# Performance work log

Measured on AMD Instinct MI355X. Metric: run time of the kernel, lower is better.

The kernel has to match this reference:

```python
import jax, jax.numpy as jnp
import numpy as np

B, L, D, H, T = 64, 512, 768, 384, 9  # batch, seq_len, hidden, hidden//2, num_tags


def setup_inputs() -> dict:
    key = jax.random.key(0)
    ks = jax.random.split(key, 8)
    return {
        "encoder_out": jax.random.normal(ks[0], (B, L, D), jnp.float32),
        "ner_labels": jax.random.randint(ks[1], (B, L), 0, T),
        "mask": jnp.ones((B, L), jnp.bool_),
        "W1": jax.random.normal(ks[2], (D, H), jnp.float32) / np.sqrt(D).astype(np.float32),
        "b1": jnp.zeros((H,), jnp.float32),
        "W2": jax.random.normal(ks[3], (H, T), jnp.float32) / np.sqrt(H).astype(np.float32),
        "b2": jnp.zeros((T,), jnp.float32),
        "start_trans": jax.random.uniform(ks[4], (T,), jnp.float32, -0.1, 0.1),
        "end_trans": jax.random.uniform(ks[5], (T,), jnp.float32, -0.1, 0.1),
        "trans": jax.random.uniform(ks[6], (T, T), jnp.float32, -0.1, 0.1),
    }


def _crf_nll(emissions, tags, mask, start_trans, end_trans, trans):
    """-mean log-likelihood, matching pytorch-crf forward (reduction='mean')."""
    maskf = mask.astype(emissions.dtype)
    # ---- numerator: score of the gold tag path ----
    emit = jnp.take_along_axis(emissions, tags[..., None], axis=-1)[..., 0]  # [B,L]
    emit_score = jnp.sum(emit * maskf, axis=1)
    tr = trans[tags[:, :-1], tags[:, 1:]]  # [B,L-1]
    tr_score = jnp.sum(tr * maskf[:, 1:], axis=1)
    last_idx = jnp.sum(mask.astype(jnp.int32), axis=1) - 1
    last_tags = jnp.take_along_axis(tags, last_idx[:, None], axis=1)[:, 0]
    numer = start_trans[tags[:, 0]] + emit_score + tr_score + end_trans[last_tags]
    # ---- denominator: forward algorithm (log partition) via scan ----
    alpha0 = start_trans[None, :] + emissions[:, 0]          # [B,T]
    em_rest = jnp.swapaxes(emissions[:, 1:], 0, 1)           # [L-1,B,T]
    mk_rest = jnp.swapaxes(maskf[:, 1:], 0, 1)               # [L-1,B]

    def step(alpha, xs):
        e_t, m_t = xs
        nxt = jax.nn.logsumexp(alpha[:, :, None] + trans[None, :, :] + e_t[:, None, :], axis=1)
        return jnp.where(m_t[:, None] > 0, nxt, alpha), None

    alpha, _ = jax.lax.scan(step, alpha0, (em_rest, mk_rest))
    denom = jax.nn.logsumexp(alpha + end_trans[None, :], axis=1)
    return -jnp.mean(numer - denom)


def reference(encoder_out, ner_labels, mask, W1, b1, W2, b2, start_trans, end_trans, trans):
    # proj: Linear -> GELU (exact erf, torch default) -> Dropout (identity in eval)
    h = jax.nn.gelu(encoder_out @ W1 + b1, approximate=False)
    emissions = h @ W2 + b2  # [B,L,T]
    return _crf_nll(emissions, ner_labels, mask, start_trans, end_trans, trans)
```

## Files before the change

### kernel.cpp

```cpp
#include <hip/hip_runtime.h>
#include <hip/hip_bf16.h>
#include <math.h>

#define B_ 64
#define L_ 512
#define D_ 768
#define H_ 384
#define T_ 9
#define M_ (B_ * L_)

typedef __attribute__((ext_vector_type(8))) short short8;
typedef __attribute__((ext_vector_type(4))) float f32x4;

__device__ __forceinline__ unsigned short f2bf(float f) {
    unsigned u = __float_as_uint(f);
    u += 0x7FFFu + ((u >> 16) & 1u);
    return (unsigned short)(u >> 16);
}

__device__ __forceinline__ unsigned pkbf2(float a, float b) {
    __hip_bfloat162 h = __float22bfloat162_rn(float2{a, b});
    return *(unsigned*)&h;
}

__device__ __forceinline__ float gelu_fast(float x) {
    float z2 = 1.5957691216f * x + 0.0713548162726f * x * x * x;
    return x / (1.f + __expf(-z2));
}

__device__ __forceinline__ float wredf(float v) {
#pragma unroll
    for (int m = 32; m >= 1; m >>= 1) v += __shfl_xor(v, m, 64);
    return v;
}

__device__ __forceinline__ void sync_lds() {
    asm volatile("s_waitcnt lgkmcnt(0)\n\ts_barrier" ::: "memory");
}

__global__ __launch_bounds__(256) void prep_kernel(
    const float* __restrict__ W1, const float* __restrict__ W2,
    unsigned short* __restrict__ W1F, unsigned short* __restrict__ W2F,
    float* __restrict__ out)
{
    if (blockIdx.x == 0 && threadIdx.x == 0) out[0] = 0.f;
    const int g    = blockIdx.x * 4 + (threadIdx.x >> 6);
    const int lane = threadIdx.x & 63;
    const int lm   = lane & 15;
    const int q    = lane >> 4;
    if (g < 576) {
        const int nt = g / 24;
        const int kc = g - nt * 24;
        const int n  = nt * 16 + lm;
        short8 v;
#pragma unroll
        for (int j = 0; j < 8; ++j)
            v[j] = (short)f2bf(W1[(size_t)(kc * 32 + q * 8 + j) * H_ + n]);
        *(short8*)(W1F + ((size_t)g * 64 + lane) * 8) = v;
    } else if (g < 588) {
        const int kk = g - 576;
        short8 v;
#pragma unroll
        for (int j = 0; j < 8; ++j) {
            int k = kk * 32 + q * 8 + j;
            v[j] = (lm < 9) ? (short)f2bf(W2[(size_t)k * T_ + lm]) : (short)0;
        }
        *(short8*)(W2F + ((size_t)kk * 64 + lane) * 8) = v;
    }
}

__global__ __launch_bounds__(256, 2) void emis_mfma_kernel(
    const float* __restrict__ X,
    const unsigned short* __restrict__ W1F,
    const float* __restrict__ b1,
    const unsigned short* __restrict__ W2F,
    const float* __restrict__ b2,
    float* __restrict__ em)
{
    __shared__ __align__(16) unsigned short Hs[64 * 392];
    char* smem = (char*)Hs;

    const int t    = threadIdx.x;
    const int lane = t & 63;
    const int w    = t >> 6;
    const int lm   = lane & 15;
    const int q    = lane >> 4;
    const int row0 = blockIdx.x * 64;

    const int srow  = t >> 2;
    const int scb   = t & 3;
    const int sslot = scb ^ ((srow >> 1) & 3);
    const float* sp = X + (size_t)(row0 + srow) * D_ + scb * 8;
    char* swr = smem + srow * 64 + sslot * 16;

    const int cq = (q ^ ((lm >> 1) & 3)) << 4;

    const unsigned short* wb = W1F + (size_t)(w * 6) * 12288 + lane * 8;

    f32x4 acc[4][6];
#pragma unroll
    for (int mt = 0; mt < 4; ++mt)
#pragma unroll
        for (int i = 0; i < 6; ++i) acc[mt][i] = (f32x4)0.f;

    short8 bb0[6], bb1[6], bb2[6];
    f32x4 gA0, gA1, gB0, gB1, gC0, gC1, gD0, gD1;

#define LOADBB(dst, KC)                                                     \
    do {                                                                    \
        dst[0] = *(const short8*)(wb + 0 * 12288 + (KC) * 512);             \
        dst[1] = *(const short8*)(wb + 1 * 12288 + (KC) * 512);             \
        dst[2] = *(const short8*)(wb + 2 * 12288 + (KC) * 512);             \
        dst[3] = *(const short8*)(wb + 3 * 12288 + (KC) * 512);             \
        dst[4] = *(const short8*)(wb + 4 * 12288 + (KC) * 512);             \
        dst[5] = *(const short8*)(wb + 5 * 12288 + (KC) * 512);             \
    } while (0)

    gA0 = *(const f32x4*)(sp);       gA1 = *(const f32x4*)(sp + 4);
    gB0 = *(const f32x4*)(sp + 32);  gB1 = *(const f32x4*)(sp + 36);
    gC0 = *(const f32x4*)(sp + 64);  gC1 = *(const f32x4*)(sp + 68);
    gD0 = *(const f32x4*)(sp + 96);  gD1 = *(const f32x4*)(sp + 100);
    LOADBB(bb0, 0);
    LOADBB(bb1, 1);
    {
        int4 v = {(int)pkbf2(gA0[0], gA0[1]), (int)pkbf2(gA0[2], gA0[3]),
                  (int)pkbf2(gA1[0], gA1[1]), (int)pkbf2(gA1[2], gA1[3])};
        *(int4*)(swr) = v;
    }
    sync_lds();

#define KSTEP(KC, BBc, BBn, Gn0, Gn1, Gw0, Gw1)                             \
    do {                                                                    \
        if ((KC) + 4 <= 23) {                                               \
            Gn0 = *(const f32x4*)(sp + ((KC) + 4) * 32);                    \
            Gn1 = *(const f32x4*)(sp + ((KC) + 4) * 32 + 4);                \
        }                                                                   \
        if ((KC) + 2 <= 23) { LOADBB(BBn, (KC) + 2); }                      \
        {                                                                   \
            const char* fb = smem + ((KC) & 1) * 4096;                      \
            short8 af0 = *(const short8*)(fb + (0 * 16 + lm) * 64 + cq);    \
            short8 af1 = *(const short8*)(fb + (1 * 16 + lm) * 64 + cq);    \
            short8 af2 = *(const short8*)(fb + (2 * 16 + lm) * 64 + cq);    \
            short8 af3 = *(const short8*)(fb + (3 * 16 + lm) * 64 + cq);    \
            acc[0][0] = __builtin_amdgcn_mfma_f32_16x16x32_bf16(af0, BBc[0], acc[0][0], 0, 0, 0); \
            acc[0][1] = __builtin_amdgcn_mfma_f32_16x16x32_bf16(af0, BBc[1], acc[0][1], 0, 0, 0); \
            acc[0][2] = __builtin_amdgcn_mfma_f32_16x16x32_bf16(af0, BBc[2], acc[0][2], 0, 0, 0); \
            acc[0][3] = __builtin_amdgcn_mfma_f32_16x16x32_bf16(af0, BBc[3], acc[0][3], 0, 0, 0); \
            acc[0][4] = __builtin_amdgcn_mfma_f32_16x16x32_bf16(af0, BBc[4], acc[0][4], 0, 0, 0); \
            acc[0][5] = __builtin_amdgcn_mfma_f32_16x16x32_bf16(af0, BBc[5], acc[0][5], 0, 0, 0); \
            acc[1][0] = __builtin_amdgcn_mfma_f32_16x16x32_bf16(af1, BBc[0], acc[1][0], 0, 0, 0); \
            acc[1][1] = __builtin_amdgcn_mfma_f32_16x16x32_bf16(af1, BBc[1], acc[1][1], 0, 0, 0); \
            acc[1][2] = __builtin_amdgcn_mfma_f32_16x16x32_bf16(af1, BBc[2], acc[1][2], 0, 0, 0); \
            acc[1][3] = __builtin_amdgcn_mfma_f32_16x16x32_bf16(af1, BBc[3], acc[1][3], 0, 0, 0); \
            acc[1][4] = __builtin_amdgcn_mfma_f32_16x16x32_bf16(af1, BBc[4], acc[1][4], 0, 0, 0); \
            acc[1][5] = __builtin_amdgcn_mfma_f32_16x16x32_bf16(af1, BBc[5], acc[1][5], 0, 0, 0); \
            acc[2][0] = __builtin_amdgcn_mfma_f32_16x16x32_bf16(af2, BBc[0], acc[2][0], 0, 0, 0); \
            acc[2][1] = __builtin_amdgcn_mfma_f32_16x16x32_bf16(af2, BBc[1], acc[2][1], 0, 0, 0); \
            acc[2][2] = __builtin_amdgcn_mfma_f32_16x16x32_bf16(af2, BBc[2], acc[2][2], 0, 0, 0); \
            acc[2][3] = __builtin_amdgcn_mfma_f32_16x16x32_bf16(af2, BBc[3], acc[2][3], 0, 0, 0); \
            acc[2][4] = __builtin_amdgcn_mfma_f32_16x16x32_bf16(af2, BBc[4], acc[2][4], 0, 0, 0); \
            acc[2][5] = __builtin_amdgcn_mfma_f32_16x16x32_bf16(af2, BBc[5], acc[2][5], 0, 0, 0); \
            acc[3][0] = __builtin_amdgcn_mfma_f32_16x16x32_bf16(af3, BBc[0], acc[3][0], 0, 0, 0); \
            acc[3][1] = __builtin_amdgcn_mfma_f32_16x16x32_bf16(af3, BBc[1], acc[3][1], 0, 0, 0); \
            acc[3][2] = __builtin_amdgcn_mfma_f32_16x16x32_bf16(af3, BBc[2], acc[3][2], 0, 0, 0); \
            acc[3][3] = __builtin_amdgcn_mfma_f32_16x16x32_bf16(af3, BBc[3], acc[3][3], 0, 0, 0); \
            acc[3][4] = __builtin_amdgcn_mfma_f32_16x16x32_bf16(af3, BBc[4], acc[3][4], 0, 0, 0); \
            acc[3][5] = __builtin_amdgcn_mfma_f32_16x16x32_bf16(af3, BBc[5], acc[3][5], 0, 0, 0); \
        }                                                                   \
        if ((KC) + 1 <= 23) {                                               \
            int4 v = {(int)pkbf2(Gw0[0], Gw0[1]), (int)pkbf2(Gw0[2], Gw0[3]), \
                      (int)pkbf2(Gw1[0], Gw1[1]), (int)pkbf2(Gw1[2], Gw1[3])}; \
            *(int4*)(swr + (((KC) + 1) & 1) * 4096) = v;                    \
            sync_lds();                                                     \
        }                                                                   \
    } while (0)

    KSTEP(  0,  bb0, bb2, gA0, gA1, gB0, gB1);
    KSTEP(  1,  bb1, bb0, gB0, gB1, gC0, gC1);
    KSTEP(  2,  bb2, bb1, gC0, gC1, gD0, gD1);
    KSTEP(  3,  bb0, bb2, gD0, gD1, gA0, gA1);
    KSTEP(  4,  bb1, bb0, gA0, gA1, gB0, gB1);
    KSTEP(  5,  bb2, bb1, gB0, gB1, gC0, gC1);
    KSTEP(  6,  bb0, bb2, gC0, gC1, gD0, gD1);
    KSTEP(  7,  bb1, bb0, gD0, gD1, gA0, gA1);
    KSTEP(  8,  bb2, bb1, gA0, gA1, gB0, gB1);
    KSTEP(  9,  bb0, bb2, gB0, gB1, gC0, gC1);
    KSTEP( 10,  bb1, bb0, gC0, gC1, gD0, gD1);
    KSTEP( 11,  bb2, bb1, gD0, gD1, gA0, gA1);
    KSTEP( 12,  bb0, bb2, gA0, gA1, gB0, gB1);
    KSTEP( 13,  bb1, bb0, gB0, gB1, gC0, gC1);
    KSTEP( 14,  bb2, bb1, gC0, gC1, gD0, gD1);
    KSTEP( 15,  bb0, bb2, gD0, gD1, gA0, gA1);
    KSTEP( 16,  bb1, bb0, gA0, gA1, gB0, gB1);
    KSTEP( 17,  bb2, bb1, gB0, gB1, gC0, gC1);
    KSTEP( 18,  bb0, bb2, gC0, gC1, gD0, gD1);
    KSTEP( 19,  bb1, bb0, gD0, gD1, gA0, gA1);
    KSTEP( 20,  bb2, bb1, gA0, gA1, gB0, gB1);
    KSTEP( 21,  bb0, bb2, gB0, gB1, gC0, gC1);
    KSTEP( 22,  bb1, bb0, gC0, gC1, gD0, gD1);
    KSTEP( 23,  bb2, bb1, gD0, gD1, gA0, gA1);

#undef KSTEP
#undef LOADBB

    __syncthreads();

#pragma unroll
    for (int i = 0; i < 6; ++i) {
        const int lc = w * 96 + i * 16 + lm;
        const float b1v = b1[lc];
#pragma unroll
        for (int mt = 0; mt < 4; ++mt)
#pragma unroll
            for (int r = 0; r < 4; ++r) {
                float h = gelu_fast(acc[mt][i][r] + b1v);
                Hs[(mt * 16 + q * 4 + r) * 392 + lc] = f2bf(h);
            }
    }
    __syncthreads();

    f32x4 e = (f32x4)0.f;
#pragma unroll
    for (int kk = 0; kk < 12; ++kk) {
        short8 ah = *(const short8*)&Hs[(w * 16 + lm) * 392 + kk * 32 + (q << 3)];
        short8 bw = *(const short8*)(W2F + ((size_t)(kk * 64 + lane)) * 8);
        e = __builtin_amdgcn_mfma_f32_16x16x32_bf16(ah, bw, e, 0, 0, 0);
    }
    if (lm < 9) {
#pragma unroll
        for (int r = 0; r < 4; ++r)
            em[(size_t)(row0 + w * 16 + q * 4 + r) * T_ + lm] = e[r] + b2[lm];
    }
}

__global__ __launch_bounds__(640) void crf_kernel(
    const float* __restrict__ em,
    const int* __restrict__ labels,
    const unsigned char* __restrict__ maskb,
    const float* __restrict__ st,
    const float* __restrict__ et,
    const float* __restrict__ tr,
    float* __restrict__ out)
{
    const int b = blockIdx.x;
    const int t = threadIdx.x;

    __shared__ float es[64 * 73];
    __shared__ float Msa[64 * 81];
    __shared__ float Msb[32 * 81];
    __shared__ float trs[81];
    __shared__ float red_num;
    __shared__ unsigned char msh[L_];
    __shared__ int lbs[L_];

    const int mstride =
        (maskb[0] != 0 && maskb[1] == 0 && maskb[2] == 0 && maskb[3] == 0) ? 4 : 1;

    const float* e0 = em + (size_t)b * L_ * T_;
    for (int i = t; i < L_ * T_; i += 640) {
        int tt = i / T_, j = i - tt * T_;
        es[(tt >> 3) * 73 + (tt & 7) * 9 + j] = e0[i];
    }
    if (t < 81) trs[t] = tr[t];
    for (int i = t; i < L_; i += 640) {
        msh[i] = maskb[((size_t)b * L_ + i) * (size_t)mstride];
        lbs[i] = labels[b * L_ + i];
    }
    __syncthreads();

    if (t < 576) {
        const int c  = t / 9;
        const int i0 = t - c * 9;
        float trr[81];
#pragma unroll
        for (int i = 0; i < 81; ++i) trr[i] = trs[i];
        float V[9];
#pragma unroll
        for (int j = 0; j < 9; ++j) V[j] = (j == i0) ? 0.f : -1e30f;

        const int sbeg = (c == 0) ? 1 : 0;
        for (int s = sbeg; s < 8; ++s) {
            int tt = c * 8 + s;
            if (msh[tt]) {
                const float* ep = &es[c * 73 + s * 9];
                float nv[9];
#pragma unroll
                for (int j = 0; j < 9; ++j) {
                    float a[9];
#pragma unroll
                    for (int k = 0; k < 9; ++k) a[k] = V[k] + trr[k * 9 + j];
                    float mx = a[0];
#pragma unroll
                    for (int k = 1; k < 9; ++k) mx = fmaxf(mx, a[k]);
                    float sum = 0.f;
#pragma unroll
                    for (int k = 0; k < 9; ++k) sum += __expf(a[k] - mx);
                    nv[j] = ep[j] + mx + __logf(sum);
                }
#pragma unroll
                for (int j = 0; j < 9; ++j) V[j] = nv[j];
            }
        }
#pragma unroll
        for (int j = 0; j < 9; ++j) Msa[c * 81 + i0 * 9 + j] = V[j];
    } else {
        const int lane = t - 576;
        float emit_s = 0.f, tr_sc = 0.f, mcnt = 0.f;
        for (int tt = lane; tt < L_; tt += 64) {
            if (msh[tt]) {
                mcnt += 1.f;
                int tag = lbs[tt];
                emit_s += es[(tt >> 3) * 73 + (tt & 7) * 9 + tag];
                if (tt >= 1) tr_sc += trs[lbs[tt - 1] * 9 + tag];
            }
        }
        emit_s = wredf(emit_s);
        tr_sc  = wredf(tr_sc);
        mcnt   = wredf(mcnt);
        if (lane == 0) {
            int last = (int)mcnt - 1;
            red_num = st[lbs[0]] + emit_s + tr_sc + et[lbs[last]];
        }
    }
    __syncthreads();

    float* src = Msa;
    float* dst = Msb;
    for (int n = 32; n >= 1; n >>= 1) {
        for (int idx = t; idx < n * 81; idx += 640) {
            int p = idx / 81;
            int r = idx - p * 81;
            int i = r / 9, j = r - i * 9;
            const float* A  = src + (2 * p) * 81 + i * 9;
            const float* Bm = src + (2 * p + 1) * 81 + j;
            float v[9];
#pragma unroll
            for (int k = 0; k < 9; ++k) v[k] = A[k] + Bm[k * 9];
            float mx = v[0];
#pragma unroll
            for (int k = 1; k < 9; ++k) mx = fmaxf(mx, v[k]);
            float sum = 0.f;
#pragma unroll
            for (int k = 0; k < 9; ++k) sum += __expf(v[k] - mx);
            dst[p * 81 + r] = mx + __logf(sum);
        }
        __syncthreads();
        float* tmp = src; src = dst; dst = tmp;
    }

    if (t < 64) {
        float v = -3.0e38f;
        if (t < 9) {
            float a[9];
#pragma unroll
            for (int i = 0; i < 9; ++i) a[i] = st[i] + es[i] + src[i * 9 + t];
            float mx = a[0];
#pragma unroll
            for (int i = 1; i < 9; ++i) mx = fmaxf(mx, a[i]);
            float sum = 0.f;
#pragma unroll
            for (int i = 0; i < 9; ++i) sum += __expf(a[i] - mx);
            v = mx + __logf(sum) + et[t];
        }
        float mx = v;
#pragma unroll
        for (int m = 32; m >= 1; m >>= 1) mx = fmaxf(mx, __shfl_xor(mx, m, 64));
        float sm = __expf(v - mx);
        sm = wredf(sm);
        if (t == 0) {
            float denom = mx + __logf(sm);
            atomicAdd(out, (denom - red_num) * (1.0f / (float)B_));
        }
    }
}

extern "C" void kernel_launch(void* const* d_in, const int* in_sizes, int n_in,
                              void* d_out, int out_size, void* d_ws, size_t ws_size,
                              hipStream_t stream) {
    const float*         enc    = (const float*)d_in[0];
    const int*           labels = (const int*)d_in[1];
    const unsigned char* mask   = (const unsigned char*)d_in[2];
    const float*         W1     = (const float*)d_in[3];
    const float*         b1     = (const float*)d_in[4];
    const float*         W2     = (const float*)d_in[5];
    const float*         b2     = (const float*)d_in[6];
    const float*         st     = (const float*)d_in[7];
    const float*         et     = (const float*)d_in[8];
    const float*         tr     = (const float*)d_in[9];

    float* em           = (float*)d_ws;
    unsigned short* W1F = (unsigned short*)(em + (size_t)M_ * T_);
    unsigned short* W2F = W1F + (size_t)576 * 64 * 8;

    prep_kernel<<<147, 256, 0, stream>>>(W1, W2, W1F, W2F, (float*)d_out);
    emis_mfma_kernel<<<512, 256, 0, stream>>>(enc, W1F, b1, W2F, b2, em);
    crf_kernel<<<B_, 640, 0, stream>>>(em, labels, mask, st, et, tr, (float*)d_out);
}
```

Baseline: 221.4 us.

## Split GEMM N-dimension across 8 waves per block instead of 4

Doubles the emission GEMM block from 256 to 512 threads so each wave computes 48 hidden columns instead of 96, halving per-wave accumulators and B-fragment registers. The X staging loads are re-split so each thread loads 4 floats per k-step, with a 3-deep prefetch ring instead of 4. The aim is more waves in flight per CU to hide memory latency. In exchange each A fragment read from LDS is reused across fewer MFMAs, LDS traffic per FLOP rises, and half the waves sit idle during the second GEMM.

```diff
diff --git a/kernel.cpp b/kernel.cpp
--- a/kernel.cpp
+++ b/kernel.cpp
@@ -69,7 +69,7 @@
     }
 }
 
-__global__ __launch_bounds__(256, 2) void emis_mfma_kernel(
+__global__ __launch_bounds__(512, 4) void emis_mfma_kernel(
     const float* __restrict__ X,
     const unsigned short* __restrict__ W1F,
     const float* __restrict__ b1,
@@ -87,127 +87,109 @@
     const int q    = lane >> 4;
     const int row0 = blockIdx.x * 64;
 
-    const int srow  = t >> 2;
-    const int scb   = t & 3;
-    const int sslot = scb ^ ((srow >> 1) & 3);
-    const float* sp = X + (size_t)(row0 + srow) * D_ + scb * 8;
-    char* swr = smem + srow * 64 + sslot * 16;
+    const int srow   = t >> 3;
+    const int slot8  = t & 7;
+    const int schunk = (slot8 >> 1) ^ ((srow >> 1) & 3);
+    const float* sp  = X + (size_t)(row0 + srow) * D_ + slot8 * 4;
+    char* swr = smem + srow * 64 + schunk * 16 + (slot8 & 1) * 8;
 
     const int cq = (q ^ ((lm >> 1) & 3)) << 4;
 
-    const unsigned short* wb = W1F + (size_t)(w * 6) * 12288 + lane * 8;
-
-    f32x4 acc[4][6];
+    const unsigned short* wb = W1F + (size_t)(w * 3) * 12288 + lane * 8;
+
+    f32x4 acc[4][3];
 #pragma unroll
     for (int mt = 0; mt < 4; ++mt)
 #pragma unroll
-        for (int i = 0; i < 6; ++i) acc[mt][i] = (f32x4)0.f;
-
-    short8 bb0[6], bb1[6], bb2[6];
-    f32x4 gA0, gA1, gB0, gB1, gC0, gC1, gD0, gD1;
+        for (int i = 0; i < 3; ++i) acc[mt][i] = (f32x4)0.f;
+
+    short8 bb0[3], bb1[3], bb2[3];
+    f32x4 g0, g1, g2;
 
 #define LOADBB(dst, KC)                                                     \
     do {                                                                    \
         dst[0] = *(const short8*)(wb + 0 * 12288 + (KC) * 512);             \
         dst[1] = *(const short8*)(wb + 1 * 12288 + (KC) * 512);             \
         dst[2] = *(const short8*)(wb + 2 * 12288 + (KC) * 512);             \
-        dst[3] = *(const short8*)(wb + 3 * 12288 + (KC) * 512);             \
-        dst[4] = *(const short8*)(wb + 4 * 12288 + (KC) * 512);             \
-        dst[5] = *(const short8*)(wb + 5 * 12288 + (KC) * 512);             \
     } while (0)
 
-    gA0 = *(const f32x4*)(sp);       gA1 = *(const f32x4*)(sp + 4);
-    gB0 = *(const f32x4*)(sp + 32);  gB1 = *(const f32x4*)(sp + 36);
-    gC0 = *(const f32x4*)(sp + 64);  gC1 = *(const f32x4*)(sp + 68);
-    gD0 = *(const f32x4*)(sp + 96);  gD1 = *(const f32x4*)(sp + 100);
+#define STWR(G, BUF)                                                        \
+    do {                                                                    \
+        int2 v2 = {(int)pkbf2(G[0], G[1]), (int)pkbf2(G[2], G[3])};         \
+        *(int2*)(swr + (BUF) * 4096) = v2;                                  \
+    } while (0)
+
+    g0 = *(const f32x4*)(sp);
+    STWR(g0, 0);
+    g1 = *(const f32x4*)(sp + 32);
+    g2 = *(const f32x4*)(sp + 64);
     LOADBB(bb0, 0);
     LOADBB(bb1, 1);
-    {
-        int4 v = {(int)pkbf2(gA0[0], gA0[1]), (int)pkbf2(gA0[2], gA0[3]),
-                  (int)pkbf2(gA1[0], gA1[1]), (int)pkbf2(gA1[2], gA1[3])};
-        *(int4*)(swr) = v;
-    }
     sync_lds();
 
-#define KSTEP(KC, BBc, BBn, Gn0, Gn1, Gw0, Gw1)                             \
+#define KSTEP(KC, BBc, BBn, Gn, Gw)                                         \
     do {                                                                    \
-        if ((KC) + 4 <= 23) {                                               \
-            Gn0 = *(const f32x4*)(sp + ((KC) + 4) * 32);                    \
-            Gn1 = *(const f32x4*)(sp + ((KC) + 4) * 32 + 4);                \
-        }                                                                   \
+        if ((KC) + 3 <= 23) Gn = *(const f32x4*)(sp + ((KC) + 3) * 32);     \
         if ((KC) + 2 <= 23) { LOADBB(BBn, (KC) + 2); }                      \
         {                                                                   \
             const char* fb = smem + ((KC) & 1) * 4096;                      \
-            short8 af0 = *(const short8*)(fb + (0 * 16 + lm) * 64 + cq);    \
-            short8 af1 = *(const short8*)(fb + (1 * 16 + lm) * 64 + cq);    \
-            short8 af2 = *(const short8*)(fb + (2 * 16 + lm) * 64 + cq);    \
-            short8 af3 = *(const short8*)(fb + (3 * 16 + lm) * 64 + cq);    \
+            short8 af0 = *(const short8*)(fb + ( 0 + lm) * 64 + cq);        \
+            short8 af1 = *(const short8*)(fb + (16 + lm) * 64 + cq);        \
+            short8 af2 = *(const short8*)(fb + (32 + lm) * 64 + cq);        \
+            short8 af3 = *(const short8*)(fb + (48 + lm) * 64 + cq);        \
             acc[0][0] = __builtin_amdgcn_mfma_f32_16x16x32_bf16(af0, BBc[0], acc[0][0], 0, 0, 0); \
             acc[0][1] = __builtin_amdgcn_mfma_f32_16x16x32_bf16(af0, BBc[1], acc[0][1], 0, 0, 0); \
             acc[0][2] = __builtin_amdgcn_mfma_f32_16x16x32_bf16(af0, BBc[2], acc[0][2], 0, 0, 0); \
-            acc[0][3] = __builtin_amdgcn_mfma_f32_16x16x32_bf16(af0, BBc[3], acc[0][3], 0, 0, 0); \
-            acc[0][4] = __builtin_amdgcn_mfma_f32_16x16x32_bf16(af0, BBc[4], acc[0][4], 0, 0, 0); \
-            acc[0][5] = __builtin_amdgcn_mfma_f32_16x16x32_bf16(af0, BBc[5], acc[0][5], 0, 0, 0); \
             acc[1][0] = __builtin_amdgcn_mfma_f32_16x16x32_bf16(af1, BBc[0], acc[1][0], 0, 0, 0); \
             acc[1][1] = __builtin_amdgcn_mfma_f32_16x16x32_bf16(af1, BBc[1], acc[1][1], 0, 0, 0); \
             acc[1][2] = __builtin_amdgcn_mfma_f32_16x16x32_bf16(af1, BBc[2], acc[1][2], 0, 0, 0); \
-            acc[1][3] = __builtin_amdgcn_mfma_f32_16x16x32_bf16(af1, BBc[3], acc[1][3], 0, 0, 0); \
-            acc[1][4] = __builtin_amdgcn_mfma_f32_16x16x32_bf16(af1, BBc[4], acc[1][4], 0, 0, 0); \
-            acc[1][5] = __builtin_amdgcn_mfma_f32_16x16x32_bf16(af1, BBc[5], acc[1][5], 0, 0, 0); \
             acc[2][0] = __builtin_amdgcn_mfma_f32_16x16x32_bf16(af2, BBc[0], acc[2][0], 0, 0, 0); \
             acc[2][1] = __builtin_amdgcn_mfma_f32_16x16x32_bf16(af2, BBc[1], acc[2][1], 0, 0, 0); \
             acc[2][2] = __builtin_amdgcn_mfma_f32_16x16x32_bf16(af2, BBc[2], acc[2][2], 0, 0, 0); \
-            acc[2][3] = __builtin_amdgcn_mfma_f32_16x16x32_bf16(af2, BBc[3], acc[2][3], 0, 0, 0); \
-            acc[2][4] = __builtin_amdgcn_mfma_f32_16x16x32_bf16(af2, BBc[4], acc[2][4], 0, 0, 0); \
-            acc[2][5] = __builtin_amdgcn_mfma_f32_16x16x32_bf16(af2, BBc[5], acc[2][5], 0, 0, 0); \
             acc[3][0] = __builtin_amdgcn_mfma_f32_16x16x32_bf16(af3, BBc[0], acc[3][0], 0, 0, 0); \
             acc[3][1] = __builtin_amdgcn_mfma_f32_16x16x32_bf16(af3, BBc[1], acc[3][1], 0, 0, 0); \
             acc[3][2] = __builtin_amdgcn_mfma_f32_16x16x32_bf16(af3, BBc[2], acc[3][2], 0, 0, 0); \
-            acc[3][3] = __builtin_amdgcn_mfma_f32_16x16x32_bf16(af3, BBc[3], acc[3][3], 0, 0, 0); \
-            acc[3][4] = __builtin_amdgcn_mfma_f32_16x16x32_bf16(af3, BBc[4], acc[3][4], 0, 0, 0); \
-            acc[3][5] = __builtin_amdgcn_mfma_f32_16x16x32_bf16(af3, BBc[5], acc[3][5], 0, 0, 0); \
         }                                                                   \
         if ((KC) + 1 <= 23) {                                               \
-            int4 v = {(int)pkbf2(Gw0[0], Gw0[1]), (int)pkbf2(Gw0[2], Gw0[3]), \
-                      (int)pkbf2(Gw1[0], Gw1[1]), (int)pkbf2(Gw1[2], Gw1[3])}; \
-            *(int4*)(swr + (((KC) + 1) & 1) * 4096) = v;                    \
+            STWR(Gw, ((KC) + 1) & 1);                                       \
             sync_lds();                                                     \
         }                                                                   \
     } while (0)
 
-    KSTEP(  0,  bb0, bb2, gA0, gA1, gB0, gB1);
-    KSTEP(  1,  bb1, bb0, gB0, gB1, gC0, gC1);
-    KSTEP(  2,  bb2, bb1, gC0, gC1, gD0, gD1);
-    KSTEP(  3,  bb0, bb2, gD0, gD1, gA0, gA1);
-    KSTEP(  4,  bb1, bb0, gA0, gA1, gB0, gB1);
-    KSTEP(  5,  bb2, bb1, gB0, gB1, gC0, gC1);
-    KSTEP(  6,  bb0, bb2, gC0, gC1, gD0, gD1);
-    KSTEP(  7,  bb1, bb0, gD0, gD1, gA0, gA1);
-    KSTEP(  8,  bb2, bb1, gA0, gA1, gB0, gB1);
-    KSTEP(  9,  bb0, bb2, gB0, gB1, gC0, gC1);
-    KSTEP( 10,  bb1, bb0, gC0, gC1, gD0, gD1);
-    KSTEP( 11,  bb2, bb1, gD0, gD1, gA0, gA1);
-    KSTEP( 12,  bb0, bb2, gA0, gA1, gB0, gB1);
-    KSTEP( 13,  bb1, bb0, gB0, gB1, gC0, gC1);
-    KSTEP( 14,  bb2, bb1, gC0, gC1, gD0, gD1);
-    KSTEP( 15,  bb0, bb2, gD0, gD1, gA0, gA1);
-    KSTEP( 16,  bb1, bb0, gA0, gA1, gB0, gB1);
-    KSTEP( 17,  bb2, bb1, gB0, gB1, gC0, gC1);
-    KSTEP( 18,  bb0, bb2, gC0, gC1, gD0, gD1);
-    KSTEP( 19,  bb1, bb0, gD0, gD1, gA0, gA1);
-    KSTEP( 20,  bb2, bb1, gA0, gA1, gB0, gB1);
-    KSTEP( 21,  bb0, bb2, gB0, gB1, gC0, gC1);
-    KSTEP( 22,  bb1, bb0, gC0, gC1, gD0, gD1);
-    KSTEP( 23,  bb2, bb1, gD0, gD1, gA0, gA1);
+    KSTEP(  0,  bb0, bb2, g0, g1);
+    KSTEP(  1,  bb1, bb0, g1, g2);
+    KSTEP(  2,  bb2, bb1, g2, g0);
+    KSTEP(  3,  bb0, bb2, g0, g1);
+    KSTEP(  4,  bb1, bb0, g1, g2);
+    KSTEP(  5,  bb2, bb1, g2, g0);
+    KSTEP(  6,  bb0, bb2, g0, g1);
+    KSTEP(  7,  bb1, bb0, g1, g2);
+    KSTEP(  8,  bb2, bb1, g2, g0);
+    KSTEP(  9,  bb0, bb2, g0, g1);
+    KSTEP( 10,  bb1, bb0, g1, g2);
+    KSTEP( 11,  bb2, bb1, g2, g0);
+    KSTEP( 12,  bb0, bb2, g0, g1);
+    KSTEP( 13,  bb1, bb0, g1, g2);
+    KSTEP( 14,  bb2, bb1, g2, g0);
+    KSTEP( 15,  bb0, bb2, g0, g1);
+    KSTEP( 16,  bb1, bb0, g1, g2);
+    KSTEP( 17,  bb2, bb1, g2, g0);
+    KSTEP( 18,  bb0, bb2, g0, g1);
+    KSTEP( 19,  bb1, bb0, g1, g2);
+    KSTEP( 20,  bb2, bb1, g2, g0);
+    KSTEP( 21,  bb0, bb2, g0, g1);
+    KSTEP( 22,  bb1, bb0, g1, g2);
+    KSTEP( 23,  bb2, bb1, g2, g0);
 
 #undef KSTEP
 #undef LOADBB
+#undef STWR
 
     __syncthreads();
 
 #pragma unroll
-    for (int i = 0; i < 6; ++i) {
-        const int lc = w * 96 + i * 16 + lm;
+    for (int i = 0; i < 3; ++i) {
+        const int lc = w * 48 + i * 16 + lm;
         const float b1v = b1[lc];
 #pragma unroll
         for (int mt = 0; mt < 4; ++mt)
@@ -219,17 +201,19 @@
     }
     __syncthreads();
 
-    f32x4 e = (f32x4)0.f;
-#pragma unroll
-    for (int kk = 0; kk < 12; ++kk) {
-        short8 ah = *(const short8*)&Hs[(w * 16 + lm) * 392 + kk * 32 + (q << 3)];
-        short8 bw = *(const short8*)(W2F + ((size_t)(kk * 64 + lane)) * 8);
-        e = __builtin_amdgcn_mfma_f32_16x16x32_bf16(ah, bw, e, 0, 0, 0);
-    }
-    if (lm < 9) {
-#pragma unroll
-        for (int r = 0; r < 4; ++r)
-            em[(size_t)(row0 + w * 16 + q * 4 + r) * T_ + lm] = e[r] + b2[lm];
+    if (w < 4) {
+        f32x4 e = (f32x4)0.f;
+#pragma unroll
+        for (int kk = 0; kk < 12; ++kk) {
+            short8 ah = *(const short8*)&Hs[(w * 16 + lm) * 392 + kk * 32 + (q << 3)];
+            short8 bw = *(const short8*)(W2F + ((size_t)(kk * 64 + lane)) * 8);
+            e = __builtin_amdgcn_mfma_f32_16x16x32_bf16(ah, bw, e, 0, 0, 0);
+        }
+        if (lm < 9) {
+#pragma unroll
+            for (int r = 0; r < 4; ++r)
+                em[(size_t)(row0 + w * 16 + q * 4 + r) * T_ + lm] = e[r] + b2[lm];
+        }
     }
 }
 
@@ -393,6 +377,6 @@
     unsigned short* W2F = W1F + (size_t)576 * 64 * 8;
 
     prep_kernel<<<147, 256, 0, stream>>>(W1, W2, W1F, W2F, (float*)d_out);
-    emis_mfma_kernel<<<512, 256, 0, stream>>>(enc, W1F, b1, W2F, b2, em);
+    emis_mfma_kernel<<<512, 512, 0, stream>>>(enc, W1F, b1, W2F, b2, em);
     crf_kernel<<<B_, 640, 0, stream>>>(em, labels, mask, st, et, tr, (float*)d_out);
 }
```

New measurement: 223.3 us. About the same (+0.9%).
